# Kernel tuning notes

Hardware: AMD Instinct MI355X
Metric: run time of the kernel (lower is better)

The kernel has to match this reference:

```python
import jax, jax.numpy as jnp
import numpy as np

B, L, D, RATIO = 256, 197, 768, 8
DK = D // RATIO  # 96


def _mk_linear(key, out_f, in_f):
    kw, kb = jax.random.split(key)
    W = jax.random.normal(kw, (out_f, in_f), jnp.float32) * 0.02  # xavier_normal gain=0.02 scale
    b = jax.random.normal(kb, (out_f,), jnp.float32) * 0.02
    return W, b


def setup_inputs() -> dict:
    key = jax.random.key(0)
    ks = jax.random.split(key, 10)
    x = jax.random.normal(ks[0], (B, L, D), jnp.float32)
    y = jax.random.normal(ks[1], (B, L, D), jnp.float32)
    Wk1, bk1 = _mk_linear(ks[2], DK, D)
    Wk2, bk2 = _mk_linear(ks[3], DK, D)
    Wks, bks = _mk_linear(ks[4], DK, DK)
    Wl1, bl1 = _mk_linear(ks[5], L, L)
    Wl2, bl2 = _mk_linear(ks[6], L, L)
    Wv1, bv1 = _mk_linear(ks[7], D, D)
    Wv2, bv2 = _mk_linear(ks[8], D, D)
    # torch inits gammas to 0; use small nonzero values so outputs/grads are non-trivial
    g = jax.random.normal(ks[9], (2,), jnp.float32) * 0.1
    gamma1 = g[:1]
    gamma2 = g[1:]
    return dict(x=x, y=y, Wk1=Wk1, bk1=bk1, Wk2=Wk2, bk2=bk2, Wks=Wks, bks=bks,
                Wl1=Wl1, bl1=bl1, Wl2=Wl2, bl2=bl2, Wv1=Wv1, bv1=bv1,
                Wv2=Wv2, bv2=bv2, gamma1=gamma1, gamma2=gamma2)


def reference(x, y, Wk1, bk1, Wk2, bk2, Wks, bks, Wl1, bl1, Wl2, bl2,
              Wv1, bv1, Wv2, bv2, gamma1, gamma2):
    b, l, d = x.shape
    # shared-projected keys (B, L, DK)
    k1 = (x @ Wk1.T + bk1) @ Wks.T + bks
    k2 = (y @ Wk2.T + bk2) @ Wks.T + bks
    # faithful to torch: .view(B, -1, L) is a raw reshape (scrambles layout), then permute
    k1r = k1.reshape(b, -1, l).swapaxes(1, 2)   # (B, L, DK)
    k2r = k2.reshape(b, -1, l)                  # (B, DK, L)
    energy = jnp.einsum('blc,bcm->blm', k1r, k2r)  # (B, L, L)
    att1 = jax.nn.softmax(energy @ Wl1.T + bl1, axis=-1)                   # att_y_on_x
    att2 = jax.nn.softmax(energy.swapaxes(1, 2) @ Wl2.T + bl2, axis=-1)    # att_x_on_y
    v2 = y @ Wv2.T + bv2  # (B, L, D)
    out_y_on_x = jnp.einsum('bdl,blm->bdm', v2.swapaxes(1, 2), att1).reshape(b, l, d)
    out_x = gamma1 * out_y_on_x + x
    v1 = x @ Wv1.T + bv1
    out_x_on_y = jnp.einsum('bdl,blm->bdm', v1.swapaxes(1, 2), att2).reshape(b, l, d)
    out_y = gamma2 * out_x_on_y + y
    return (out_x, out_y)
```

## Files before the change

kernel.cpp:

```cpp
#include <hip/hip_runtime.h>
#include <math.h>

typedef unsigned short ushort;
typedef __attribute__((ext_vector_type(4))) unsigned short bfx4;
typedef __attribute__((ext_vector_type(8))) short short8;
typedef __attribute__((ext_vector_type(8))) unsigned short ushort8;
typedef __attribute__((ext_vector_type(4))) float f32x4;
typedef unsigned int u32;

#define VM_WAIT(N) asm volatile("s_waitcnt vmcnt(" #N ")" ::: "memory")
#define LGKM_WAIT() asm volatile("s_waitcnt lgkmcnt(0)" ::: "memory")
#define SBAR() asm volatile("s_barrier" ::: "memory")

__device__ __forceinline__ int swz4(int row) {
  return (row & 3) ^ ((row >> 2) & 3);
}

__device__ __forceinline__ ushort f2bf(float f) {
  u32 u = __float_as_uint(f);
  return (ushort)((u + 0x7FFF + ((u >> 16) & 1)) >> 16);
}
__device__ __forceinline__ float bf2f(ushort u) {
  u32 v = ((u32)u) << 16;
  return __uint_as_float(v);
}

__device__ __forceinline__ void gload16(const void* g, void* l) {
  __builtin_amdgcn_global_load_lds(
      (const __attribute__((address_space(1))) u32*)g,
      (__attribute__((address_space(3))) u32*)l, 16, 0, 0);
}

#define BKK 32
#define LDSP 68
__global__ __launch_bounds__(256) void gemm_generic(
    const float* __restrict__ A, const float* __restrict__ Bm, const float* __restrict__ Bm2,
    float* __restrict__ C, float* __restrict__ C2,
    int M, int N, int K, long sAi, long sAk, long sBj, long sBk, long sCi)
{
  __shared__ __align__(16) float lds_a[BKK * LDSP];
  __shared__ __align__(16) float lds_b[BKK * LDSP];
  const float* Bb = blockIdx.z ? Bm2 : Bm;
  float* Cc = blockIdx.z ? C2 : C;
  const int i0 = blockIdx.y * 64;
  const int j0 = blockIdx.x * 64;
  const int tid = threadIdx.x;
  const int tx = tid & 15, ty = tid >> 4;
  float acc[4][4] = {};
  for (int k0 = 0; k0 < K; k0 += BKK) {
    for (int idx = tid; idx < BKK * 64; idx += 256) {
      int kk = idx & (BKK - 1), ii = idx >> 5;
      int gi = i0 + ii, gk = k0 + kk;
      lds_a[kk * LDSP + ii] = (gi < M && gk < K) ? A[(long)gi * sAi + (long)gk * sAk] : 0.f;
    }
    for (int idx = tid; idx < BKK * 64; idx += 256) {
      int kk = idx & (BKK - 1), jj = idx >> 5;
      int gj = j0 + jj, gk = k0 + kk;
      lds_b[kk * LDSP + jj] = (gj < N && gk < K) ? Bb[(long)gj * sBj + (long)gk * sBk] : 0.f;
    }
    __syncthreads();
    #pragma unroll
    for (int kk = 0; kk < BKK; ++kk) {
      const float4 a4 = *reinterpret_cast<const float4*>(&lds_a[kk * LDSP + ty * 4]);
      const float4 b4 = *reinterpret_cast<const float4*>(&lds_b[kk * LDSP + tx * 4]);
      const float av[4] = {a4.x, a4.y, a4.z, a4.w};
      const float bv[4] = {b4.x, b4.y, b4.z, b4.w};
      #pragma unroll
      for (int a = 0; a < 4; ++a)
        #pragma unroll
        for (int b = 0; b < 4; ++b)
          acc[a][b] = fmaf(av[a], bv[b], acc[a][b]);
    }
    __syncthreads();
  }
  for (int a = 0; a < 4; ++a) {
    int gi = i0 + ty * 4 + a;
    if (gi >= M) continue;
    for (int b = 0; b < 4; ++b) {
      int gj = j0 + tx * 4 + b;
      if (gj >= N) continue;
      Cc[(long)gi * sCi + gj] = acc[a][b];
    }
  }
}

__global__ __launch_bounds__(256) void mfma_gemm(
    const ushort* __restrict__ A0, const ushort* __restrict__ A1,
    const ushort* __restrict__ B0, const ushort* __restrict__ B1,
    const float* __restrict__ bias0, const float* __restrict__ bias1,
    ushort* __restrict__ C0, ushort* __restrict__ C1,
    int M, int N, int K, long sAi, long sBj, long sCi)
{
  __shared__ ushort As[128 * 64];
  __shared__ ushort Bs[128 * 64];
  const int which = blockIdx.z;
  const ushort* Ab = which ? A1 : A0;
  const ushort* Bb = which ? B1 : B0;
  const float* bias = which ? bias1 : bias0;
  ushort* C = which ? C1 : C0;
  const int i0 = blockIdx.y * 128;
  const int j0 = blockIdx.x * 128;
  const int tid = threadIdx.x;
  const int wave = tid >> 6, lane = tid & 63;
  const int wm = wave >> 1, wn = wave & 1;
  const int col16 = lane & 15, krow = lane >> 4;

  f32x4 acc[4][4] = {};

  for (int k0 = 0; k0 < K; k0 += 64) {
    #pragma unroll
    for (int it = 0; it < 4; ++it) {
      int chunk = it * 256 + wave * 64 + lane;
      int row = chunk >> 3, s = chunk & 7;
      int kc = s ^ (row & 7);
      int gi = i0 + row; if (gi >= M) gi = M - 1;
      gload16(Ab + (long)gi * sAi + k0 + kc * 8, &As[chunk * 8]);
    }
    #pragma unroll
    for (int it = 0; it < 4; ++it) {
      int chunk = it * 256 + wave * 64 + lane;
      int row = chunk >> 3, s = chunk & 7;
      int kc = s ^ (row & 7);
      int gj = j0 + row; if (gj >= N) gj = N - 1;
      gload16(Bb + (long)gj * sBj + k0 + kc * 8, &Bs[chunk * 8]);
    }
    __syncthreads();
    #pragma unroll
    for (int ks = 0; ks < 2; ++ks) {
      short8 af[4], bfr[4];
      #pragma unroll
      for (int mi = 0; mi < 4; ++mi) {
        int row = wm * 64 + mi * 16 + col16;
        int slot = (ks * 4 + krow) ^ (row & 7);
        af[mi] = *(const short8*)&As[row * 64 + slot * 8];
      }
      #pragma unroll
      for (int nj = 0; nj < 4; ++nj) {
        int row = wn * 64 + nj * 16 + col16;
        int slot = (ks * 4 + krow) ^ (row & 7);
        bfr[nj] = *(const short8*)&Bs[row * 64 + slot * 8];
      }
      #pragma unroll
      for (int mi = 0; mi < 4; ++mi)
        #pragma unroll
        for (int nj = 0; nj < 4; ++nj)
          acc[mi][nj] = __builtin_amdgcn_mfma_f32_16x16x32_bf16(
              af[mi], bfr[nj], acc[mi][nj], 0, 0, 0);
    }
    __syncthreads();
  }

  const int r0 = krow * 4;
  #pragma unroll
  for (int mi = 0; mi < 4; ++mi) {
    int gi0 = i0 + wm * 64 + mi * 16 + r0;
    #pragma unroll
    for (int nj = 0; nj < 4; ++nj) {
      int gj = j0 + wn * 64 + nj * 16 + col16;
      f32x4 a = acc[mi][nj];
      #pragma unroll
      for (int r = 0; r < 4; ++r) {
        int gi = gi0 + r;
        if (gi >= M || gj >= N) continue;
        C[(long)gi * sCi + gj] = f2bf(a[r] + bias[gj]);
      }
    }
  }
}

__global__ __launch_bounds__(256) void transpose_k(
    const ushort* __restrict__ k1, const ushort* __restrict__ k2,
    ushort* __restrict__ EA1, ushort* __restrict__ EA2, int Bc)
{
  __shared__ ushort tile[32][33];
  int z = blockIdx.z;
  int which = (z >= Bc) ? 1 : 0;
  int b = which ? z - Bc : z;
  const ushort* src = (which ? k2 : k1) + (long)b * 18912;
  ushort* dst = (which ? EA2 : EA1) + (long)b * 25216;
  int l0 = blockIdx.x * 32, c0 = blockIdx.y * 32;
  int tx = threadIdx.x & 31, ty = threadIdx.x >> 5;
  for (int r = ty; r < 32; r += 8) {
    int c = c0 + r, l = l0 + tx;
    tile[r][tx] = (c < 96 && l < 197) ? src[(long)c * 197 + l] : (ushort)0;
  }
  __syncthreads();
  for (int r = ty; r < 32; r += 8) {
    int l = l0 + r, c = c0 + tx;
    if (l < 197 && c < 128) dst[(long)l * 128 + c] = tile[tx][r];
  }
}

__global__ __launch_bounds__(256) void energy_mfma(
    const ushort* __restrict__ EA1, const ushort* __restrict__ EA2,
    ushort* __restrict__ Eb, ushort* __restrict__ ETb)
{
  __shared__ ushort elds[16896];
  ushort* As = elds;
  ushort* Bs = elds + 8192;
  const int bz = blockIdx.z;
  const ushort* Ab = EA1 + 25216L * bz;
  const ushort* Bb = EA2 + 25216L * bz;
  const int i0 = blockIdx.y * 128;
  const int j0 = blockIdx.x * 128;
  const int tid = threadIdx.x;
  const int wave = tid >> 6, lane = tid & 63;
  const int wm = wave >> 1, wn = wave & 1;
  const int col16 = lane & 15, krow = lane >> 4;

  f32x4 acc[4][4] = {};

  for (int k0 = 0; k0 < 128; k0 += 64) {
    #pragma unroll
    for (int it = 0; it < 4; ++it) {
      int chunk = it * 256 + wave * 64 + lane;
      int row = chunk >> 3, s = chunk & 7;
      int kc = s ^ (row & 7);
      int gi = i0 + row; if (gi > 196) gi = 196;
      gload16(Ab + (long)gi * 128 + k0 + kc * 8, &As[chunk * 8]);
    }
    #pragma unroll
    for (int it = 0; it < 4; ++it) {
      int chunk = it * 256 + wave * 64 + lane;
      int row = chunk >> 3, s = chunk & 7;
      int kc = s ^ (row & 7);
      int gj = j0 + row; if (gj > 196) gj = 196;
      gload16(Bb + (long)gj * 128 + k0 + kc * 8, &Bs[chunk * 8]);
    }
    __syncthreads();
    #pragma unroll
    for (int ks = 0; ks < 2; ++ks) {
      short8 af[4], bfr[4];
      #pragma unroll
      for (int mi = 0; mi < 4; ++mi) {
        int row = wm * 64 + mi * 16 + col16;
        int slot = (ks * 4 + krow) ^ (row & 7);
        af[mi] = *(const short8*)&As[row * 64 + slot * 8];
      }
      #pragma unroll
      for (int nj = 0; nj < 4; ++nj) {
        int row = wn * 64 + nj * 16 + col16;
        int slot = (ks * 4 + krow) ^ (row & 7);
        bfr[nj] = *(const short8*)&Bs[row * 64 + slot * 8];
      }
      #pragma unroll
      for (int mi = 0; mi < 4; ++mi)
        #pragma unroll
        for (int nj = 0; nj < 4; ++nj)
          acc[mi][nj] = __builtin_amdgcn_mfma_f32_16x16x32_bf16(
              af[mi], bfr[nj], acc[mi][nj], 0, 0, 0);
    }
    __syncthreads();
  }

  ushort* obufT = elds;
  #pragma unroll
  for (int mi = 0; mi < 4; ++mi)
    #pragma unroll
    for (int nj = 0; nj < 4; ++nj) {
      int mcol = wn * 64 + nj * 16 + col16;
      int lrow = wm * 64 + mi * 16 + krow * 4;
      bfx4 h;
      #pragma unroll
      for (int r = 0; r < 4; ++r) h[r] = f2bf(acc[mi][nj][r]);
      *(bfx4*)&obufT[mcol * 132 + lrow] = h;
    }
  SBAR();
  {
    int lL = tid & 63, mg = tid >> 6;
    for (int it = 0; it < 32; ++it) {
      int mL = mg * 32 + it;
      int gm = j0 + mL;
      if (gm >= 197) break;
      #pragma unroll
      for (int lh = 0; lh < 2; ++lh) {
        int l = lh * 64 + lL;
        int gl = i0 + l;
        if (gl < 224)
          ETb[bz * 50432L + (long)gm * 256 + gl] =
              (gl < 197) ? obufT[mL * 132 + l] : (ushort)0;
      }
    }
  }
  {
    int mL = tid & 63, lg = tid >> 6;
    for (int it = 0; it < 32; ++it) {
      int lL = lg * 32 + it;
      int gl = i0 + lL;
      if (gl >= 197) break;
      #pragma unroll
      for (int mh = 0; mh < 2; ++mh) {
        int m = mh * 64 + mL;
        int gm = j0 + m;
        if (gm < 224)
          Eb[bz * 50432L + (long)gl * 256 + gm] =
              (gm < 197) ? obufT[m * 132 + lL] : (ushort)0;
      }
    }
  }
}

__global__ __launch_bounds__(256) void att_gemm(
    const ushort* __restrict__ Wl0, const ushort* __restrict__ Wl1,
    const ushort* __restrict__ E0, const ushort* __restrict__ E1,
    const float* __restrict__ bl0, const float* __restrict__ bl1,
    ushort* __restrict__ a0, ushort* __restrict__ a1out)
{
  __shared__ ushort Aws[2][208 * 32];
  __shared__ ushort Bws[2][64 * 32];
  __shared__ float blds[208];
  const int which = blockIdx.z;
  const int bz = blockIdx.y;
  const ushort* Wl = which ? Wl1 : Wl0;
  const ushort* Bb = (which ? E1 : E0) + 50432L * bz;
  const float* bl = which ? bl1 : bl0;
  ushort* aout = which ? a1out : a0;
  const int l0 = blockIdx.x * 64;
  const int tid = threadIdx.x, wave = tid >> 6, lane = tid & 63;
  const int col16 = lane & 15, kq = lane >> 4;

  if (tid < 208) blds[tid] = (tid < 197) ? bl[tid] : 0.f;

  f32x4 acc[13] = {};

  auto stage = [&](int buf, int k0) {
    const int lrow = lane >> 2, s = lane & 3;
    #pragma unroll
    for (int c0 = 0; c0 < 5; ++c0) {
      int c = wave + c0 * 4;
      if (c >= 17) break;
      if (c < 13) {
        int row = c * 16 + lrow;
        int gr = row < 197 ? row : 196;
        int kc = s ^ swz4(row);
        gload16(Wl + (long)gr * 256 + k0 + kc * 8,
                (char*)(&Aws[buf][0]) + c * 1024 + lane * 16);
      } else {
        int row = (c - 13) * 16 + lrow;
        int gl = l0 + row; if (gl > 196) gl = 196;
        int kc = s ^ swz4(row);
        gload16(Bb + (long)gl * 256 + k0 + kc * 8,
                (char*)(&Bws[buf][0]) + (c - 13) * 1024 + lane * 16);
      }
    }
  };

  stage(0, 0);
  for (int t = 0; t < 7; ++t) {
    int cur = t & 1;
    if (t + 1 < 7) {
      stage(cur ^ 1, (t + 1) * 32);
      if (wave == 0) VM_WAIT(5); else VM_WAIT(4);
    } else {
      VM_WAIT(0);
    }
    SBAR();
    int brow = wave * 16 + col16;
    short8 bf = *(const short8*)((const char*)(&Bws[cur][0]) +
                                 brow * 64 + ((kq ^ swz4(brow)) << 4));
    #pragma unroll
    for (int j = 0; j < 13; ++j) {
      int arow = j * 16 + col16;
      short8 af = *(const short8*)((const char*)(&Aws[cur][0]) +
                                   arow * 64 + ((kq ^ swz4(arow)) << 4));
      acc[j] = __builtin_amdgcn_mfma_f32_16x16x32_bf16(af, bf, acc[j], 0, 0, 0);
    }
    SBAR();
  }

  const int c = l0 + wave * 16 + col16;
  float mx = -INFINITY;
  #pragma unroll
  for (int j = 0; j < 13; ++j)
    #pragma unroll
    for (int r = 0; r < 4; ++r) {
      int m = j * 16 + kq * 4 + r;
      float v = acc[j][r] + blds[m];
      v = (m < 197) ? v : -INFINITY;
      acc[j][r] = v;
      mx = fmaxf(mx, v);
    }
  mx = fmaxf(mx, __shfl_xor(mx, 16));
  mx = fmaxf(mx, __shfl_xor(mx, 32));
  float s = 0.f;
  #pragma unroll
  for (int j = 0; j < 13; ++j)
    #pragma unroll
    for (int r = 0; r < 4; ++r) {
      int m = j * 16 + kq * 4 + r;
      float e = (m < 197) ? __expf(acc[j][r] - mx) : 0.f;
      acc[j][r] = e;
      s += e;
    }
  s += __shfl_xor(s, 16);
  s += __shfl_xor(s, 32);
  const float inv = 1.f / s;
  ushort* ab = aout + 50432L * bz;
  #pragma unroll
  for (int j = 0; j < 13; ++j)
    #pragma unroll
    for (int r = 0; r < 4; ++r) {
      int m = j * 16 + kq * 4 + r;
      if (m < 197)
        ab[(long)m * 256 + c] = (c < 197) ? f2bf(acc[j][r] * inv) : (ushort)0;
    }
}

__global__ __launch_bounds__(256) void vfused_gemm(
    const ushort* __restrict__ Wv0, const ushort* __restrict__ Wv1,
    const ushort* __restrict__ S0, const ushort* __restrict__ S1,
    const float* __restrict__ bv0, const float* __restrict__ bv1,
    const ushort* __restrict__ At0, const ushort* __restrict__ At1,
    const ushort* __restrict__ R0, const ushort* __restrict__ R1,
    const float* __restrict__ g0, const float* __restrict__ g1,
    float* __restrict__ C0, float* __restrict__ C1,
    int Bc)
{
  __shared__ __align__(16) char lds[58368];
  const int per = 12 * Bc;
  int bid = blockIdx.x;
  const int which = bid / per;
  bid -= which * per;
  int dtile, b;
  if ((Bc & 7) == 0) {
    int xcd = bid & 7, sid = bid >> 3;
    dtile = sid % 12;
    b = (sid / 12) * 8 + xcd;
  } else {
    dtile = bid % 12;
    b = bid / 12;
  }
  const ushort* Wv = (which ? Wv1 : Wv0) + (long)(dtile * 64) * 768;
  const ushort* Sb = (which ? S1 : S0) + (long)b * 197 * 768;
  const float* bv = which ? bv1 : bv0;
  const ushort* attb = (which ? At1 : At0) + (long)b * 50432;
  const ushort* resid = which ? R1 : R0;
  const float g = (which ? g1 : g0)[0];
  float* C = which ? C1 : C0;

  const int tid = threadIdx.x, wave = tid >> 6, lane = tid & 63;
  const int wr = wave >> 1, wc = wave & 1;
  const int col16 = lane & 15, kq = lane >> 4;

  f32x4 acc[2][7] = {};

  auto stage1 = [&](int buf, int k0) {
    const int lrow = lane >> 2, s = lane & 3;
    #pragma unroll
    for (int c0 = 0; c0 < 5; ++c0) {
      int c = wave + c0 * 4;
      if (c >= 18) break;
      if (c < 4) {
        int row = c * 16 + lrow;
        int kc = s ^ swz4(row);
        gload16(Wv + (long)row * 768 + k0 + kc * 8,
                lds + buf * 4096 + c * 1024 + lane * 16);
      } else {
        int j = (c - 4) * 16 + lrow;
        int gr = j < 197 ? j : 196;
        int kc = s ^ swz4(j);
        gload16(Sb + (long)gr * 768 + k0 + kc * 8,
                lds + 8192 + buf * 14336 + (c - 4) * 1024 + lane * 16);
      }
    }
  };

  stage1(0, 0);
  for (int t = 0; t < 24; ++t) {
    int cur = t & 1;
    if (t + 1 < 24) {
      stage1(cur ^ 1, (t + 1) << 5);
      if (wave < 2) VM_WAIT(5); else VM_WAIT(4);
    } else {
      VM_WAIT(0);
    }
    SBAR();
    short8 af[2];
    #pragma unroll
    for (int mi = 0; mi < 2; ++mi) {
      int ar = wr * 32 + mi * 16 + col16;
      af[mi] = *(const short8*)(lds + cur * 4096 + ar * 64 + ((kq ^ swz4(ar)) << 4));
    }
    #pragma unroll
    for (int nj = 0; nj < 7; ++nj) {
      int br = wc * 112 + nj * 16 + col16;
      short8 bf = *(const short8*)(lds + 8192 + cur * 14336 +
                                   br * 64 + ((kq ^ swz4(br)) << 4));
      #pragma unroll
      for (int mi = 0; mi < 2; ++mi)
        acc[mi][nj] = __builtin_amdgcn_mfma_f32_16x16x32_bf16(
            af[mi], bf, acc[mi][nj], 0, 0, 0);
    }
    SBAR();
  }

  ushort* vlds = (ushort*)(lds + 28672);
  #pragma unroll
  for (int mi = 0; mi < 2; ++mi)
    #pragma unroll
    for (int r = 0; r < 4; ++r) {
      int dl = wr * 32 + mi * 16 + kq * 4 + r;
      float bvv = bv[dtile * 64 + dl];
      #pragma unroll
      for (int nj = 0; nj < 7; ++nj) {
        int l = wc * 112 + nj * 16 + col16;
        vlds[dl * 232 + l] = f2bf(acc[mi][nj][r] + bvv);
      }
    }
  LGKM_WAIT();
  SBAR();

  #pragma unroll
  for (int mi = 0; mi < 2; ++mi)
    #pragma unroll
    for (int nj = 0; nj < 7; ++nj)
      acc[mi][nj] = (f32x4){0.f, 0.f, 0.f, 0.f};

  auto stage2 = [&](int buf, int k0) {
    const int lrow = lane >> 2, s = lane & 3;
    #pragma unroll
    for (int c0 = 0; c0 < 4; ++c0) {
      int c = wave + c0 * 4;
      if (c >= 14) break;
      int m = c * 16 + lrow;
      int gm = m < 197 ? m : 196;
      int kc = s ^ swz4(m);
      gload16(attb + (long)gm * 256 + k0 + kc * 8,
              lds + buf * 14336 + c * 1024 + lane * 16);
    }
  };

  stage2(0, 0);
  for (int t = 0; t < 7; ++t) {
    int cur = t & 1;
    if (t + 1 < 7) {
      stage2(cur ^ 1, (t + 1) << 5);
      if (wave < 2) VM_WAIT(4); else VM_WAIT(3);
    } else {
      VM_WAIT(0);
    }
    SBAR();
    const int k0 = t << 5;
    short8 af[2];
    #pragma unroll
    for (int mi = 0; mi < 2; ++mi) {
      int ar = wr * 32 + mi * 16 + col16;
      af[mi] = *(const short8*)((const char*)vlds + ar * 464 + k0 * 2 + kq * 16);
    }
    #pragma unroll
    for (int nj = 0; nj < 7; ++nj) {
      int br = wc * 112 + nj * 16 + col16;
      short8 bf = *(const short8*)(lds + cur * 14336 +
                                   br * 64 + ((kq ^ swz4(br)) << 4));
      #pragma unroll
      for (int mi = 0; mi < 2; ++mi)
        acc[mi][nj] = __builtin_amdgcn_mfma_f32_16x16x32_bf16(
            af[mi], bf, acc[mi][nj], 0, 0, 0);
    }
    SBAR();
  }

  ushort* obufT = (ushort*)lds;
  #pragma unroll 1
  for (int c = 0; c < 2; ++c) {
    if (wc == c) {
      #pragma unroll
      for (int mi = 0; mi < 2; ++mi)
        #pragma unroll
        for (int nj = 0; nj < 7; ++nj) {
          int colL = nj * 16 + col16;
          int row = wr * 32 + mi * 16 + kq * 4;
          bfx4 h;
          #pragma unroll
          for (int r = 0; r < 4; ++r) h[r] = f2bf(g * acc[mi][nj][r]);
          *(bfx4*)&obufT[colL * 68 + row] = h;
        }
    }
    SBAR();
    {
      int colL = tid & 127, rg = tid >> 7;
      int ncols = 197 - c * 112; if (ncols > 112) ncols = 112;
      if (colL < ncols) {
        int gcol = c * 112 + colL;
        #pragma unroll 4
        for (int it = 0; it < 32; ++it) {
          int row = rg * 32 + it;
          long ci = (long)b * 151296 + (long)(dtile * 64 + row) * 197 + gcol;
          C[ci] = bf2f(obufT[colL * 68 + row]) + bf2f(resid[ci]);
        }
      }
    }
    SBAR();
  }
}

__global__ void fuse_bias2(const float* __restrict__ Wks,
                           const float* __restrict__ bk1, const float* __restrict__ bk2,
                           const float* __restrict__ bks,
                           float* __restrict__ bf1, float* __restrict__ bf2) {
  int c = threadIdx.x;
  if (c >= 192) return;
  const float* bk = (c < 96) ? bk1 : bk2;
  float* bf = (c < 96) ? bf1 : bf2;
  int cc = (c < 96) ? c : c - 96;
  float s = bks[cc];
  for (int e = 0; e < 96; ++e) s += Wks[cc * 96 + e] * bk[e];
  bf[cc] = s;
}

__global__ __launch_bounds__(256) void conv_weights(
    const float* __restrict__ Wf1, const float* __restrict__ Wf2,
    const float* __restrict__ Wv1, const float* __restrict__ Wv2,
    const float* __restrict__ Wl1, const float* __restrict__ Wl2,
    ushort* __restrict__ Wf1b, ushort* __restrict__ Wf2b,
    ushort* __restrict__ Wv1b, ushort* __restrict__ Wv2b,
    ushort* __restrict__ Wl1b, ushort* __restrict__ Wl2b)
{
  const long total = 147456 + 1179648 + 100864;
  long stride = (long)gridDim.x * blockDim.x;
  for (long i = (long)blockIdx.x * blockDim.x + threadIdx.x; i < total; i += stride) {
    if (i < 147456) {
      long j = i;
      if (j < 73728) Wf1b[j] = f2bf(Wf1[j]);
      else Wf2b[j - 73728] = f2bf(Wf2[j - 73728]);
    } else if (i < 147456 + 1179648) {
      long j = i - 147456;
      if (j < 589824) Wv1b[j] = f2bf(Wv1[j]);
      else Wv2b[j - 589824] = f2bf(Wv2[j - 589824]);
    } else {
      long j = i - 147456 - 1179648;
      int w2 = j >= 50432;
      if (w2) j -= 50432;
      int r = (int)(j >> 8), cc = (int)(j & 255);
      const float* s = w2 ? Wl2 : Wl1;
      ushort* d = w2 ? Wl2b : Wl1b;
      d[j] = (cc < 197) ? f2bf(s[(long)r * 197 + cc]) : (ushort)0;
    }
  }
}

__global__ __launch_bounds__(256) void conv_xy(const float* __restrict__ x,
                                               const float* __restrict__ y,
                                               ushort* __restrict__ xb,
                                               ushort* __restrict__ yb, long n8) {
  long i = (long)blockIdx.x * blockDim.x + threadIdx.x;
  long stride = (long)gridDim.x * blockDim.x;
  for (; i < 2 * n8; i += stride) {
    const float* s = (i < n8) ? x : y;
    ushort* d = (i < n8) ? xb : yb;
    long j = (i < n8) ? i : i - n8;
    float4 a = ((const float4*)s)[2 * j];
    float4 b = ((const float4*)s)[2 * j + 1];
    ushort8 o;
    o[0] = f2bf(a.x); o[1] = f2bf(a.y); o[2] = f2bf(a.z); o[3] = f2bf(a.w);
    o[4] = f2bf(b.x); o[5] = f2bf(b.y); o[6] = f2bf(b.z); o[7] = f2bf(b.w);
    *(ushort8*)&d[j * 8] = o;
  }
}

extern "C" void kernel_launch(void* const* d_in, const int* in_sizes, int n_in,
                              void* d_out, int out_size, void* d_ws, size_t ws_size,
                              hipStream_t stream) {
  const float* x   = (const float*)d_in[0];
  const float* y   = (const float*)d_in[1];
  const float* Wk1 = (const float*)d_in[2];
  const float* bk1 = (const float*)d_in[3];
  const float* Wk2 = (const float*)d_in[4];
  const float* bk2 = (const float*)d_in[5];
  const float* Wks = (const float*)d_in[6];
  const float* bks = (const float*)d_in[7];
  const float* Wl1 = (const float*)d_in[8];
  const float* bl1 = (const float*)d_in[9];
  const float* Wl2 = (const float*)d_in[10];
  const float* bl2 = (const float*)d_in[11];
  const float* Wv1 = (const float*)d_in[12];
  const float* bv1 = (const float*)d_in[13];
  const float* Wv2 = (const float*)d_in[14];
  const float* bv2 = (const float*)d_in[15];
  const float* gamma1 = (const float*)d_in[16];
  const float* gamma2 = (const float*)d_in[17];
  float* out = (float*)d_out;

  const int B = 256, L = 197, D = 768;
  const long LD = (long)L * D;

  const size_t staticBytes = 3446784;
  const size_t perB = 605184 + 75648 + 100864 + 201728 + 201728;
  int Bc = 256;
  while (Bc > 8 && staticBytes + (size_t)Bc * perB > ws_size) Bc >>= 1;

  char* p = (char*)d_ws;
  auto carve = [&](size_t bytes) { char* r = p; p += bytes; return r; };
  float*  Wf1   = (float*)carve(73728 * 4);
  float*  Wf2   = (float*)carve(73728 * 4);
  float*  bf1   = (float*)carve(512);
  float*  bf2   = (float*)carve(512);
  ushort* Wv1b  = (ushort*)carve(589824 * 2);
  ushort* Wv2b  = (ushort*)carve(589824 * 2);
  ushort* Wf1b  = (ushort*)carve(73728 * 2);
  ushort* Wf2b  = (ushort*)carve(73728 * 2);
  ushort* Wl1b  = (ushort*)carve(50432 * 2);
  ushort* Wl2b  = (ushort*)carve(50432 * 2);
  ushort* xb    = (ushort*)carve((size_t)Bc * LD * 2);
  ushort* yb    = (ushort*)carve((size_t)Bc * LD * 2);
  ushort* k1    = (ushort*)carve((size_t)Bc * 18912 * 2);
  ushort* k2    = (ushort*)carve((size_t)Bc * 18912 * 2);
  ushort* EA1   = (ushort*)carve((size_t)Bc * 25216 * 2);
  ushort* EA2   = (ushort*)carve((size_t)Bc * 25216 * 2);
  ushort* Eb    = (ushort*)carve((size_t)Bc * 50432 * 2);
  ushort* ETbuf = (ushort*)carve((size_t)Bc * 50432 * 2);
  ushort* a1    = (ushort*)carve((size_t)Bc * 50432 * 2);
  ushort* a2    = (ushort*)carve((size_t)Bc * 50432 * 2);

  dim3 blk(256);

  gemm_generic<<<dim3(12, 2, 2), blk, 0, stream>>>(Wks, Wk1, Wk2, Wf1, Wf2,
      96, 768, 96, 96, 1, 1, 768, 768);
  fuse_bias2<<<1, 192, 0, stream>>>(Wks, bk1, bk2, bks, bf1, bf2);
  conv_weights<<<dim3(1024), blk, 0, stream>>>(Wf1, Wf2, Wv1, Wv2, Wl1, Wl2,
      Wf1b, Wf2b, Wv1b, Wv2b, Wl1b, Wl2b);

  for (int c0 = 0; c0 < B; c0 += Bc) {
    const float* xc = x + (long)c0 * LD;
    const float* yc = y + (long)c0 * LD;
    const int Mr = Bc * L;
    const int gym = (Mr + 127) / 128;

    conv_xy<<<dim3(2048), blk, 0, stream>>>(xc, yc, xb, yb, (long)Bc * LD / 8);

    mfma_gemm<<<dim3(1, gym, 2), blk, 0, stream>>>(xb, yb, Wf1b, Wf2b, bf1, bf2,
        k1, k2, Mr, 96, 768, 768, 768, 96);

    transpose_k<<<dim3(7, 4, 2 * Bc), blk, 0, stream>>>(k1, k2, EA1, EA2, Bc);

    energy_mfma<<<dim3(2, 2, Bc), blk, 0, stream>>>(EA1, EA2, Eb, ETbuf);

    att_gemm<<<dim3(4, Bc, 2), blk, 0, stream>>>(Wl1b, Wl2b, Eb, ETbuf,
        bl1, bl2, a1, a2);

    vfused_gemm<<<dim3(2 * 12 * Bc), blk, 0, stream>>>(
        Wv2b, Wv1b, yb, xb, bv2, bv1, a1, a2, xb, yb, gamma1, gamma2,
        out + (long)c0 * LD, out + (long)B * LD + (long)c0 * LD, Bc);
  }
}
```

Measured before the change: 636.7 us.

## Single-buffer attention stage in vfused_gemm to shrink LDS footprint

Removes the double-buffered prefetch of attention tiles in the second GEMM stage of vfused_gemm, loading each K-slice synchronously into one buffer. This cuts shared memory from 58368 to 44032 bytes, presumably so more blocks fit per CU. Hand-written s_barrier/waitcnt pairs are replaced with __syncthreads. The cost is that the global-to-LDS load latency is no longer overlapped with MFMA work in that loop.

```diff
diff --git a/kernel.cpp b/kernel.cpp
--- a/kernel.cpp
+++ b/kernel.cpp
@@ -9,7 +9,6 @@
 typedef unsigned int u32;
 
 #define VM_WAIT(N) asm volatile("s_waitcnt vmcnt(" #N ")" ::: "memory")
-#define LGKM_WAIT() asm volatile("s_waitcnt lgkmcnt(0)" ::: "memory")
 #define SBAR() asm volatile("s_barrier" ::: "memory")
 
 __device__ __forceinline__ int swz4(int row) {
@@ -265,7 +264,7 @@
       for (int r = 0; r < 4; ++r) h[r] = f2bf(acc[mi][nj][r]);
       *(bfx4*)&obufT[mcol * 132 + lrow] = h;
     }
-  SBAR();
+  __syncthreads();
   {
     int lL = tid & 63, mg = tid >> 6;
     for (int it = 0; it < 32; ++it) {
@@ -416,7 +415,7 @@
     float* __restrict__ C0, float* __restrict__ C1,
     int Bc)
 {
-  __shared__ __align__(16) char lds[58368];
+  __shared__ __align__(16) char lds[44032];
   const int per = 12 * Bc;
   int bid = blockIdx.x;
   const int which = bid / per;
@@ -493,8 +492,9 @@
     }
     SBAR();
   }
-
-  ushort* vlds = (ushort*)(lds + 28672);
+  __syncthreads();
+
+  ushort* vlds = (ushort*)(lds + 14336);
   #pragma unroll
   for (int mi = 0; mi < 2; ++mi)
     #pragma unroll
@@ -507,8 +507,7 @@
         vlds[dl * 232 + l] = f2bf(acc[mi][nj][r] + bvv);
       }
     }
-  LGKM_WAIT();
-  SBAR();
+  __syncthreads();
 
   #pragma unroll
   for (int mi = 0; mi < 2; ++mi)
@@ -516,7 +515,7 @@
     for (int nj = 0; nj < 7; ++nj)
       acc[mi][nj] = (f32x4){0.f, 0.f, 0.f, 0.f};
 
-  auto stage2 = [&](int buf, int k0) {
+  auto stage2 = [&](int k0) {
     const int lrow = lane >> 2, s = lane & 3;
     #pragma unroll
     for (int c0 = 0; c0 < 4; ++c0) {
@@ -526,20 +525,13 @@
       int gm = m < 197 ? m : 196;
       int kc = s ^ swz4(m);
       gload16(attb + (long)gm * 256 + k0 + kc * 8,
-              lds + buf * 14336 + c * 1024 + lane * 16);
+              lds + c * 1024 + lane * 16);
     }
   };
 
-  stage2(0, 0);
   for (int t = 0; t < 7; ++t) {
-    int cur = t & 1;
-    if (t + 1 < 7) {
-      stage2(cur ^ 1, (t + 1) << 5);
-      if (wave < 2) VM_WAIT(4); else VM_WAIT(3);
-    } else {
-      VM_WAIT(0);
-    }
-    SBAR();
+    stage2(t << 5);
+    __syncthreads();
     const int k0 = t << 5;
     short8 af[2];
     #pragma unroll
@@ -550,14 +542,13 @@
     #pragma unroll
     for (int nj = 0; nj < 7; ++nj) {
       int br = wc * 112 + nj * 16 + col16;
-      short8 bf = *(const short8*)(lds + cur * 14336 +
-                                   br * 64 + ((kq ^ swz4(br)) << 4));
+      short8 bf = *(const short8*)(lds + br * 64 + ((kq ^ swz4(br)) << 4));
       #pragma unroll
       for (int mi = 0; mi < 2; ++mi)
         acc[mi][nj] = __builtin_amdgcn_mfma_f32_16x16x32_bf16(
             af[mi], bf, acc[mi][nj], 0, 0, 0);
     }
-    SBAR();
+    __syncthreads();
   }
 
   ushort* obufT = (ushort*)lds;
@@ -576,7 +567,7 @@
           *(bfx4*)&obufT[colL * 68 + row] = h;
         }
     }
-    SBAR();
+    __syncthreads();
     {
       int colL = tid & 127, rg = tid >> 7;
       int ncols = 197 - c * 112; if (ncols > 112) ncols = 112;
@@ -590,7 +581,7 @@
         }
       }
     }
-    SBAR();
+    __syncthreads();
   }
 }
 
```

Result: faster. 603.9 us (median of 3 runs) (-5.2%).
